# Optimization experiments

Measured on AMD Instinct MI355X. Metric: run time of the kernel, lower is better.

The kernel has to match this reference:

```python
import jax, jax.numpy as jnp
import numpy as np

N = 100000
NLAYERS = 4
NPROP = 2
NGRAPHS = 50


def gcn_conv(x, edge_index, W, b):
    """PyG GCNConv: h = x@W; out[d] = sum_e norm_e * h[src_e] (+ self loops), norm = D^-1/2 A_hat D^-1/2."""
    n = x.shape[0]
    loop = jnp.arange(n, dtype=edge_index.dtype)
    src = jnp.concatenate([edge_index[0], loop])
    dst = jnp.concatenate([edge_index[1], loop])
    deg = jax.ops.segment_sum(jnp.ones(src.shape[0], x.dtype), dst, num_segments=n)
    dinv = jax.lax.rsqrt(deg)  # deg >= 1 thanks to self loops
    norm = (dinv[src] * dinv[dst])[:, None]
    h = x @ W
    return jax.ops.segment_sum(h[src] * norm, dst, num_segments=n) + b


def setup_inputs() -> dict:
    key = jax.random.key(0)
    ks = jax.random.split(key, 16)
    inp = {
        "x": jax.random.normal(ks[0], (N, 16), jnp.float32),
        "feature_mtx_static": jax.random.normal(ks[1], (N, 32), jnp.float32),
        "edge_index": jax.random.randint(ks[2], (2, 400000), 0, N, jnp.int32),
        "inner_edges": jax.random.randint(ks[3], (NLAYERS, 2, 300000), 0, N, jnp.int32),
        "forward_edges": jax.random.randint(ks[4], (NLAYERS, 2, 300000), 0, N, jnp.int32),
        "backward_edges": jax.random.randint(ks[5], (NLAYERS, 2, 300000), 0, N, jnp.int32),
        "layers": jax.random.randint(ks[6], (N,), 0, NLAYERS, jnp.int32),
        "batch": jnp.sort(jax.random.randint(ks[7], (N,), 0, NGRAPHS, jnp.int32)),
        "W_up": jax.random.normal(ks[8], (16, 256), jnp.float32) * 0.25,
        "b_up": jax.random.normal(ks[9], (256,), jnp.float32) * 0.02,
        "W_in": jax.random.normal(ks[10], (288, 256), jnp.float32) * 0.06,
        "b_in": jax.random.normal(ks[11], (256,), jnp.float32) * 0.02,
        "W_fw": jax.random.normal(ks[12], (288, 256), jnp.float32) * 0.06,
        "b_fw": jax.random.normal(ks[13], (256,), jnp.float32) * 0.02,
        "W_lin": jax.random.normal(ks[14], (256, 1), jnp.float32) * 0.06,
        "b_lin": jax.random.normal(ks[15], (1,), jnp.float32) * 0.02,
    }
    return inp


def reference(x, feature_mtx_static, edge_index, inner_edges, forward_edges,
              backward_edges, layers, batch, W_up, b_up, W_in, b_in,
              W_fw, b_fw, W_lin, b_lin):
    def addstatic(h):
        return jnp.concatenate([h, feature_mtx_static], axis=1)

    x = gcn_conv(x, edge_index, W_up, b_up)
    partial_inner = x  # placeholder; overwritten in forward sweep
    for _ in range(NPROP):
        for il in range(NLAYERS):
            layermask = layers == il
            partial_inner = gcn_conv(addstatic(x), inner_edges[il], W_in, b_in)
            x = jnp.where(layermask[:, None], partial_inner, x)
            next_layer_mask = layers == il + 1
            partial_forward = gcn_conv(addstatic(x), forward_edges[il], W_fw, b_fw)
            x = jnp.where(next_layer_mask[:, None], partial_forward, x)
        x = jax.nn.relu(x)
        for il in range(NLAYERS - 1, -1, -1):
            # NOTE: original code computes forward_conv on backward_edges here but
            # assigns from the stale `partial_inner` (dead compute skipped).
            previous_layer_mask = layers == il - 1
            x = jnp.where(previous_layer_mask[:, None], partial_inner, x)
            layermask = layers == il
            partial_backward = gcn_conv(addstatic(x), inner_edges[il], W_in, b_in)
            x = jnp.where(layermask[:, None], partial_backward, x)
        x = jax.nn.relu(x)

    pooled = jax.ops.segment_sum(x, batch, num_segments=NGRAPHS)  # [G, 256]
    return pooled @ W_lin + b_lin  # [G, 1]
```

## Files before the change

### kernel.cpp

```cpp
#include <hip/hip_runtime.h>

#define N_NODES 100000
#define NLAYERS 4
#define NPROP 2
#define NGRAPHS 50
#define NE_MAIN 400000
#define NE_SET 300000
#define NSETS 9
#define CSR_TOTAL (NE_MAIN + 8 * NE_SET)
#define ASTR 296
#define WFSZ (9 * 16 * 512)
#define PCHUNK 4096
#define NCHK 25

typedef __attribute__((ext_vector_type(8))) short bf8_t;
typedef __attribute__((ext_vector_type(8))) unsigned short us8_t;
typedef __attribute__((ext_vector_type(4))) float f4_t;

__device__ __align__(16) unsigned short g_x[(size_t)N_NODES * 256];
__device__ __align__(16) unsigned short g_pi[(size_t)N_NODES * 256];
__device__ __align__(16) unsigned short g_fsb[(size_t)N_NODES * 32];
__device__ __align__(16) float g_agg16[(size_t)N_NODES * 16];
__device__ __align__(16) float g_dinv[NSETS * N_NODES];
__device__ __align__(16) float g_pooled[NGRAPHS * 256];
__device__ __align__(16) unsigned short g_Wfh[2 * WFSZ];
__device__ __align__(16) unsigned short g_Wfl[2 * WFSZ];
__device__ int g_deg[NSETS * N_NODES];
__device__ int g_cur[NSETS * N_NODES];
__device__ int g_off[NSETS * (N_NODES + 1)];
__device__ int g_part[NSETS * NCHK];
__device__ int g_csrs[CSR_TOTAL];
__device__ int g_cnt[4];
__device__ int g_lists[NLAYERS * N_NODES];

__host__ __device__ inline int csr_base(int slot) {
    return slot == 0 ? 0 : NE_MAIN + (slot - 1) * NE_SET;
}

__device__ inline unsigned short f2bf(float f) {
    unsigned u = __float_as_uint(f);
    return (unsigned short)((u + 0x7fffu + ((u >> 16) & 1u)) >> 16);
}
__device__ inline float bf2f(unsigned short b) {
    return __uint_as_float(((unsigned)b) << 16);
}

__device__ inline void edge_decode(int t, const int* ei, const int* inner, const int* fwd,
                                   int& slot, const int*& es, const int*& ed, int& e) {
    if (t < NE_MAIN) {
        slot = 0; e = t; es = ei; ed = ei + NE_MAIN;
    } else {
        int r = t - NE_MAIN;
        int grp = r / NE_SET;
        e = r - grp * NE_SET;
        slot = 1 + grp;
        const int* base = (grp < 4) ? (inner + grp * 2 * NE_SET)
                                    : (fwd + (grp - 4) * 2 * NE_SET);
        es = base; ed = base + NE_SET;
    }
}


__global__ __launch_bounds__(256) void k_init() {
    int i = blockIdx.x * blockDim.x + threadIdx.x;
    if (i < NSETS * N_NODES) g_deg[i] = 0;
    if (i < NGRAPHS * 256) g_pooled[i] = 0.f;
    if (i < 4) g_cnt[i] = 0;
}

__global__ __launch_bounds__(256) void k_fsb(const float* __restrict__ fs) {
    int i = blockIdx.x * blockDim.x + threadIdx.x;
    if (i < N_NODES * 32) g_fsb[i] = f2bf(fs[i]);
}

__global__ __launch_bounds__(256) void k_count_all(const int* __restrict__ ei,
                                                   const int* __restrict__ inner,
                                                   const int* __restrict__ fwd) {
    int t = blockIdx.x * blockDim.x + threadIdx.x;
    if (t >= CSR_TOTAL) return;
    int slot, e; const int *es, *ed;
    edge_decode(t, ei, inner, fwd, slot, es, ed, e);
    atomicAdd(&g_deg[slot * N_NODES + ed[e]], 1);
}

__global__ __launch_bounds__(256) void k_dinv() {
    int i = blockIdx.x * blockDim.x + threadIdx.x;
    if (i < NSETS * N_NODES) g_dinv[i] = rsqrtf(1.0f + (float)g_deg[i]);
}

__global__ __launch_bounds__(256) void k_wt(const float* __restrict__ W, int which) {
    int t = blockIdx.x * blockDim.x + threadIdx.x;
    if (t >= 288 * 256) return;
    int k = t >> 8, n = t & 255;
    int kb = k >> 5, kq = k & 31, quad = kq >> 3, ke = kq & 7;
    int nt = n >> 4, m = n & 15, lane = quad * 16 + m;
    int idx = which * WFSZ + (kb * 16 + nt) * 512 + lane * 8 + ke;
    float w = W[t];
    unsigned short h = f2bf(w);
    unsigned short l = f2bf(w - bf2f(h));
    g_Wfh[idx] = h;
    g_Wfl[idx] = l;
}


__global__ __launch_bounds__(256) void k_scan_a() {
    int b = blockIdx.x;
    int set = b / NCHK, ch = b % NCHK;
    const int* deg = g_deg + (size_t)set * N_NODES;
    int base = ch * PCHUNK + threadIdx.x * 16;
    int s = 0;
#pragma unroll
    for (int j = 0; j < 16; j++) {
        int id = base + j;
        if (id < N_NODES) s += deg[id];
    }
    __shared__ int sm[256];
    sm[threadIdx.x] = s;
    __syncthreads();
    for (int o = 128; o > 0; o >>= 1) {
        if (threadIdx.x < o) sm[threadIdx.x] += sm[threadIdx.x + o];
        __syncthreads();
    }
    if (threadIdx.x == 0) g_part[b] = sm[0];
}

__global__ __launch_bounds__(1024) void k_scan_b() {
    int wv = threadIdx.x >> 6, lane = threadIdx.x & 63;
    if (wv >= NSETS) return;
    int v = (lane < NCHK) ? g_part[wv * NCHK + lane] : 0;
    int orig = v;
    for (int o = 1; o < 32; o <<= 1) {
        int u = __shfl_up(v, o);
        if (lane >= o) v += u;
    }
    if (lane < NCHK) g_part[wv * NCHK + lane] = v - orig;
}

__global__ __launch_bounds__(256) void k_scan_c() {
    int b = blockIdx.x;
    int set = b / NCHK, ch = b % NCHK;
    const int* deg = g_deg + (size_t)set * N_NODES;
    int* off = g_off + (size_t)set * (N_NODES + 1);
    int* cur = g_cur + (size_t)set * N_NODES;
    int t = threadIdx.x;
    int base = ch * PCHUNK + t * 16;
    int v[16];
    int s = 0;
#pragma unroll
    for (int j = 0; j < 16; j++) {
        int id = base + j;
        v[j] = (id < N_NODES) ? deg[id] : 0;
        s += v[j];
    }
    __shared__ int sm[256];
    sm[t] = s;
    __syncthreads();
    for (int o = 1; o < 256; o <<= 1) {
        int u = (t >= o) ? sm[t - o] : 0;
        __syncthreads();
        sm[t] += u;
        __syncthreads();
    }
    int run = g_part[b] + sm[t] - s;
#pragma unroll
    for (int j = 0; j < 16; j++) {
        int id = base + j;
        if (id < N_NODES) { off[id] = run; cur[id] = run; }
        run += v[j];
    }
    if (ch == NCHK - 1 && t == 255) off[N_NODES] = (set == 0) ? NE_MAIN : NE_SET;
}

__global__ __launch_bounds__(256) void k_fill_all(const int* __restrict__ ei,
                                                  const int* __restrict__ inner,
                                                  const int* __restrict__ fwd) {
    int t = blockIdx.x * blockDim.x + threadIdx.x;
    if (t >= CSR_TOTAL) return;
    int slot, e; const int *es, *ed;
    edge_decode(t, ei, inner, fwd, slot, es, ed, e);
    int s = es[e], d = ed[e];
    int pos = atomicAdd(&g_cur[slot * N_NODES + d], 1);
    g_csrs[csr_base(slot) + pos] = s;
}

__global__ __launch_bounds__(256) void k_lists(const int* __restrict__ layers) {
    __shared__ int lcnt[4];
    __shared__ int lbase[4];
    int i = blockIdx.x * blockDim.x + threadIdx.x;
    if (threadIdx.x < 4) lcnt[threadIdx.x] = 0;
    __syncthreads();
    int l = -1, p = 0;
    if (i < N_NODES) {
        l = layers[i];
        p = atomicAdd(&lcnt[l], 1);
    }
    __syncthreads();
    if (threadIdx.x < 4) lbase[threadIdx.x] = atomicAdd(&g_cnt[threadIdx.x], lcnt[threadIdx.x]);
    __syncthreads();
    if (l >= 0) g_lists[l * N_NODES + lbase[l] + p] = i;
}


__global__ __launch_bounds__(256) void k_gather16(const float* __restrict__ xin) {
    int g = blockIdx.x * blockDim.x + threadIdx.x;
    int i = g >> 4, lane = g & 15;
    if (i >= N_NODES) return;
    float dv = g_dinv[i];
    float acc = dv * dv * xin[i * 16 + lane];
    int e0 = g_off[i], e1 = g_off[i + 1];
    for (int e = e0; e < e1; e++) {
        int s = g_csrs[e];
        acc += g_dinv[s] * dv * xin[s * 16 + lane];
    }
    g_agg16[i * 16 + lane] = acc;
}

__global__ __launch_bounds__(256) void k_gemm0(const float* __restrict__ W,
                                               const float* __restrict__ bias) {
    __shared__ float a[128];
    int base = blockIdx.x * 8;
    int t = threadIdx.x;
    if (t < 128) a[t] = g_agg16[base * 16 + t];
    __syncthreads();
    float bb = bias[t];
    for (int r = 0; r < 8; r++) {
        float acc = bb;
#pragma unroll
        for (int k = 0; k < 16; k++) acc += a[r * 16 + k] * W[k * 256 + t];
        g_x[(size_t)(base + r) * 256 + t] = f2bf(acc);
    }
}


__global__ __launch_bounds__(256, 4) void k_conv(int slot, int which,
                                                 const float* __restrict__ bias,
                                                 const int* __restrict__ layersp,
                                                 int layer, int topi) {
    int count = (layer >= 0) ? g_cnt[layer] : N_NODES;
    int base = blockIdx.x * 32;
    if (base >= count) return;
    const unsigned short* Wfh = g_Wfh + (size_t)which * WFSZ;
    const unsigned short* Wfl = g_Wfl + (size_t)which * WFSZ;
    unsigned short* out = topi ? g_pi : g_x;

    __shared__ unsigned short lds_h[32 * ASTR];
    __shared__ unsigned short lds_l[32 * ASTR];
    __shared__ int rows_s[32];
    int t = threadIdx.x;
    if (t < 32) {
        int r = base + t;
        rows_s[t] = (r < count) ? ((layer >= 0) ? g_lists[layer * N_NODES + r] : r) : -1;
    }
    __syncthreads();

    int wv = t >> 6, lane = t & 63;
    int grp = lane >> 4, gl = lane & 15;

    const float* dinv_s = g_dinv + (size_t)slot * N_NODES;
    const int* offp = g_off + (size_t)slot * (N_NODES + 1);
    int cb = csr_base(slot);
    for (int rr = 0; rr < 2; rr++) {
        int lr = wv * 8 + grp * 2 + rr;
        int row = rows_s[lr];
        float acc0[8], acc1[8], accf[8];
#pragma unroll
        for (int j = 0; j < 8; j++) { acc0[j] = 0.f; acc1[j] = 0.f; accf[j] = 0.f; }
        if (row >= 0) {
            float dvr = dinv_s[row];
            float d2 = dvr * dvr;
            us8_t u0 = *(const us8_t*)&g_x[(size_t)row * 256 + gl * 8];
            us8_t u1 = *(const us8_t*)&g_x[(size_t)row * 256 + 128 + gl * 8];
#pragma unroll
            for (int j = 0; j < 8; j++) { acc0[j] = d2 * bf2f(u0[j]); acc1[j] = d2 * bf2f(u1[j]); }
            if (gl < 4) {
                us8_t uf = *(const us8_t*)&g_fsb[(size_t)row * 32 + gl * 8];
#pragma unroll
                for (int j = 0; j < 8; j++) accf[j] = d2 * bf2f(uf[j]);
            }
            int e0 = offp[row] + cb, e1e = offp[row + 1] + cb;
            int e = e0;
            for (; e + 1 < e1e; e += 2) {
                int sa = g_csrs[e], sb = g_csrs[e + 1];
                float na = dinv_s[sa] * dvr;
                float nb = dinv_s[sb] * dvr;
                us8_t va0 = *(const us8_t*)&g_x[(size_t)sa * 256 + gl * 8];
                us8_t va1 = *(const us8_t*)&g_x[(size_t)sa * 256 + 128 + gl * 8];
                us8_t vb0 = *(const us8_t*)&g_x[(size_t)sb * 256 + gl * 8];
                us8_t vb1 = *(const us8_t*)&g_x[(size_t)sb * 256 + 128 + gl * 8];
#pragma unroll
                for (int j = 0; j < 8; j++) {
                    acc0[j] += na * bf2f(va0[j]); acc1[j] += na * bf2f(va1[j]);
                    acc0[j] += nb * bf2f(vb0[j]); acc1[j] += nb * bf2f(vb1[j]);
                }
                if (gl < 4) {
                    us8_t fa = *(const us8_t*)&g_fsb[(size_t)sa * 32 + gl * 8];
                    us8_t fb = *(const us8_t*)&g_fsb[(size_t)sb * 32 + gl * 8];
#pragma unroll
                    for (int j = 0; j < 8; j++)
                        accf[j] += na * bf2f(fa[j]) + nb * bf2f(fb[j]);
                }
            }
            if (e < e1e) {
                int sa = g_csrs[e];
                float na = dinv_s[sa] * dvr;
                us8_t va0 = *(const us8_t*)&g_x[(size_t)sa * 256 + gl * 8];
                us8_t va1 = *(const us8_t*)&g_x[(size_t)sa * 256 + 128 + gl * 8];
#pragma unroll
                for (int j = 0; j < 8; j++) {
                    acc0[j] += na * bf2f(va0[j]); acc1[j] += na * bf2f(va1[j]);
                }
                if (gl < 4) {
                    us8_t fa = *(const us8_t*)&g_fsb[(size_t)sa * 32 + gl * 8];
#pragma unroll
                    for (int j = 0; j < 8; j++) accf[j] += na * bf2f(fa[j]);
                }
            }
        }
        us8_t h0, l0, h1, l1;
#pragma unroll
        for (int j = 0; j < 8; j++) {
            h0[j] = f2bf(acc0[j]); l0[j] = f2bf(acc0[j] - bf2f(h0[j]));
            h1[j] = f2bf(acc1[j]); l1[j] = f2bf(acc1[j] - bf2f(h1[j]));
        }
        *(us8_t*)&lds_h[lr * ASTR + gl * 8] = h0;
        *(us8_t*)&lds_h[lr * ASTR + 128 + gl * 8] = h1;
        *(us8_t*)&lds_l[lr * ASTR + gl * 8] = l0;
        *(us8_t*)&lds_l[lr * ASTR + 128 + gl * 8] = l1;
        if (gl < 4) {
            us8_t hf, lf;
#pragma unroll
            for (int j = 0; j < 8; j++) {
                hf[j] = f2bf(accf[j]); lf[j] = f2bf(accf[j] - bf2f(hf[j]));
            }
            *(us8_t*)&lds_h[lr * ASTR + 256 + gl * 8] = hf;
            *(us8_t*)&lds_l[lr * ASTR + 256 + gl * 8] = lf;
        }
    }
    __syncthreads();

    int m = lane & 15, quad = lane >> 4;
    int n0 = wv * 64;
    f4_t acc2[2][4];
#pragma unroll
    for (int rt = 0; rt < 2; rt++)
#pragma unroll
        for (int ct = 0; ct < 4; ct++) acc2[rt][ct] = (f4_t){0.f, 0.f, 0.f, 0.f};

    for (int kb = 0; kb < 9; kb++) {
        int k0 = kb * 32;
        bf8_t ah0 = *(const bf8_t*)&lds_h[m * ASTR + k0 + quad * 8];
        bf8_t al0 = *(const bf8_t*)&lds_l[m * ASTR + k0 + quad * 8];
        bf8_t ah1 = *(const bf8_t*)&lds_h[(16 + m) * ASTR + k0 + quad * 8];
        bf8_t al1 = *(const bf8_t*)&lds_l[(16 + m) * ASTR + k0 + quad * 8];
#pragma unroll
        for (int ct = 0; ct < 4; ct++) {
            int nt = wv * 4 + ct;
            const bf8_t bh = *(const bf8_t*)&Wfh[(kb * 16 + nt) * 512 + lane * 8];
            const bf8_t bl = *(const bf8_t*)&Wfl[(kb * 16 + nt) * 512 + lane * 8];
            acc2[0][ct] = __builtin_amdgcn_mfma_f32_16x16x32_bf16(ah0, bh, acc2[0][ct], 0, 0, 0);
            acc2[0][ct] = __builtin_amdgcn_mfma_f32_16x16x32_bf16(al0, bh, acc2[0][ct], 0, 0, 0);
            acc2[0][ct] = __builtin_amdgcn_mfma_f32_16x16x32_bf16(ah0, bl, acc2[0][ct], 0, 0, 0);
            acc2[1][ct] = __builtin_amdgcn_mfma_f32_16x16x32_bf16(ah1, bh, acc2[1][ct], 0, 0, 0);
            acc2[1][ct] = __builtin_amdgcn_mfma_f32_16x16x32_bf16(al1, bh, acc2[1][ct], 0, 0, 0);
            acc2[1][ct] = __builtin_amdgcn_mfma_f32_16x16x32_bf16(ah1, bl, acc2[1][ct], 0, 0, 0);
        }
    }
#pragma unroll
    for (int rt = 0; rt < 2; rt++) {
#pragma unroll
        for (int r = 0; r < 4; r++) {
            int row = rows_s[rt * 16 + quad * 4 + r];
            if (row < 0) continue;
            int dual = topi && (layersp[row] == 3);
#pragma unroll
            for (int ct = 0; ct < 4; ct++) {
                int n = n0 + ct * 16 + m;
                unsigned short v = f2bf(acc2[rt][ct][r] + bias[n]);
                out[(size_t)row * 256 + n] = v;
                if (dual) g_x[(size_t)row * 256 + n] = v;
            }
        }
    }
}


__global__ __launch_bounds__(256) void k_copy_rows(int layer) {
    int w = (blockIdx.x * blockDim.x + threadIdx.x) >> 5;
    int lane = threadIdx.x & 31;
    if (w >= g_cnt[layer]) return;
    int i = g_lists[layer * N_NODES + w];
    *(uint4*)(g_x + (size_t)i * 256 + lane * 8) =
        *(const uint4*)(g_pi + (size_t)i * 256 + lane * 8);
}

__global__ __launch_bounds__(256) void k_relu() {
    int i = blockIdx.x * blockDim.x + threadIdx.x;
    if (i >= N_NODES * 32) return;
    ushort4 a = ((ushort4*)g_x)[i * 2];
    ushort4 b = ((ushort4*)g_x)[i * 2 + 1];
    a.x = (a.x & 0x8000) ? 0 : a.x; a.y = (a.y & 0x8000) ? 0 : a.y;
    a.z = (a.z & 0x8000) ? 0 : a.z; a.w = (a.w & 0x8000) ? 0 : a.w;
    b.x = (b.x & 0x8000) ? 0 : b.x; b.y = (b.y & 0x8000) ? 0 : b.y;
    b.z = (b.z & 0x8000) ? 0 : b.z; b.w = (b.w & 0x8000) ? 0 : b.w;
    ((ushort4*)g_x)[i * 2] = a;
    ((ushort4*)g_x)[i * 2 + 1] = b;
}

__global__ __launch_bounds__(256) void k_pool(const int* __restrict__ batch) {
    __shared__ int bs[128];
    int i0 = blockIdx.x * 128;
    if (threadIdx.x < 128) {
        int i = i0 + threadIdx.x;
        bs[threadIdx.x] = (i < N_NODES) ? batch[i] : -1;
    }
    __syncthreads();
    int c = threadIdx.x;
    int lim = min(128, N_NODES - i0);
    float acc = 0.f;
    int cur = bs[0];
    for (int ii = 0; ii < lim; ii++) {
        int g = bs[ii];
        if (g != cur) { atomicAdd(&g_pooled[cur * 256 + c], acc); acc = 0.f; cur = g; }
        acc += fmaxf(bf2f(g_x[(size_t)(i0 + ii) * 256 + c]), 0.f);
    }
    atomicAdd(&g_pooled[cur * 256 + c], acc);
}

__global__ void k_final(const float* __restrict__ W_lin, const float* __restrict__ b_lin,
                        float* __restrict__ out) {
    int g = blockIdx.x;
    int lane = threadIdx.x;
    float4 p = *(const float4*)(g_pooled + g * 256 + lane * 4);
    float4 w = *(const float4*)(W_lin + lane * 4);
    float s = p.x * w.x + p.y * w.y + p.z * w.z + p.w * w.w;
    for (int o = 32; o > 0; o >>= 1) s += __shfl_down(s, o);
    if (lane == 0) out[g] = s + b_lin[0];
}


extern "C" void kernel_launch(void* const* d_in, const int* in_sizes, int n_in,
                              void* d_out, int out_size, void* d_ws, size_t ws_size,
                              hipStream_t stream) {
    const float* xin   = (const float*)d_in[0];
    const float* fs    = (const float*)d_in[1];
    const int* ei      = (const int*)d_in[2];
    const int* inner   = (const int*)d_in[3];
    const int* fwd     = (const int*)d_in[4];
    const int* layers  = (const int*)d_in[6];
    const int* batch   = (const int*)d_in[7];
    const float* W_up  = (const float*)d_in[8];
    const float* b_up  = (const float*)d_in[9];
    const float* W_in  = (const float*)d_in[10];
    const float* b_in  = (const float*)d_in[11];
    const float* W_fw  = (const float*)d_in[12];
    const float* b_fw  = (const float*)d_in[13];
    const float* W_lin = (const float*)d_in[14];
    const float* b_lin = (const float*)d_in[15];
    float* out = (float*)d_out;

    k_init<<<(NSETS * N_NODES + 255) / 256, 256, 0, stream>>>();
    k_fsb<<<(N_NODES * 32 + 255) / 256, 256, 0, stream>>>(fs);
    k_wt<<<(288 * 256 + 255) / 256, 256, 0, stream>>>(W_in, 0);
    k_wt<<<(288 * 256 + 255) / 256, 256, 0, stream>>>(W_fw, 1);
    k_count_all<<<(CSR_TOTAL + 255) / 256, 256, 0, stream>>>(ei, inner, fwd);
    k_dinv<<<(NSETS * N_NODES + 255) / 256, 256, 0, stream>>>();
    k_scan_a<<<NSETS * NCHK, 256, 0, stream>>>();
    k_scan_b<<<1, 1024, 0, stream>>>();
    k_scan_c<<<NSETS * NCHK, 256, 0, stream>>>();
    k_fill_all<<<(CSR_TOTAL + 255) / 256, 256, 0, stream>>>(ei, inner, fwd);
    k_lists<<<(N_NODES + 255) / 256, 256, 0, stream>>>(layers);

    k_gather16<<<(N_NODES * 16 + 255) / 256, 256, 0, stream>>>(xin);
    k_gemm0<<<N_NODES / 8, 256, 0, stream>>>(W_up, b_up);

    auto conv = [&](int slot, int which, const float* bias, int layer, int topi) {
        k_conv<<<(N_NODES + 31) / 32, 256, 0, stream>>>(slot, which, bias, layers, layer, topi);
    };

    for (int p = 0; p < NPROP; p++) {
        for (int il = 0; il < NLAYERS; il++) {
            if (il < NLAYERS - 1) {
                conv(1 + il, 0, b_in, il, 0);
                conv(5 + il, 1, b_fw, il + 1, 0);
            } else {
                conv(1 + il, 0, b_in, -1, 1);
            }
        }
        k_relu<<<(N_NODES * 32 + 255) / 256, 256, 0, stream>>>();
        for (int il = NLAYERS - 1; il >= 0; il--) {
            if (il >= 1) k_copy_rows<<<12500, 256, 0, stream>>>(il - 1);
            conv(1 + il, 0, b_in, il, 0);
        }
        if (p < NPROP - 1)
            k_relu<<<(N_NODES * 32 + 255) / 256, 256, 0, stream>>>();
    }

    k_pool<<<(N_NODES + 127) / 128, 256, 0, stream>>>(batch);
    k_final<<<NGRAPHS, 64, 0, stream>>>(W_lin, b_lin, out);
}
```

Baseline: 1.508 ms.

## Build filtered CSR containing only edges for destination rows actually consumed

```diff
diff --git a/kernel.cpp b/kernel.cpp
--- a/kernel.cpp
+++ b/kernel.cpp
@@ -26,6 +26,7 @@
 __device__ __align__(16) unsigned short g_Wfh[2 * WFSZ];
 __device__ __align__(16) unsigned short g_Wfl[2 * WFSZ];
 __device__ int g_deg[NSETS * N_NODES];
+__device__ int g_degf[NSETS * N_NODES];
 __device__ int g_cur[NSETS * N_NODES];
 __device__ int g_off[NSETS * (N_NODES + 1)];
 __device__ int g_part[NSETS * NCHK];
@@ -60,10 +61,17 @@
     }
 }
 
+__device__ inline int csr_keep(int slot, int ld) {
+    if (slot == 0 || slot == 4) return 1;
+    if (slot <= 3) return ld == slot - 1;
+    if (slot <= 7) return ld == slot - 4;
+    return 0;
+}
+
 
 __global__ __launch_bounds__(256) void k_init() {
     int i = blockIdx.x * blockDim.x + threadIdx.x;
-    if (i < NSETS * N_NODES) g_deg[i] = 0;
+    if (i < NSETS * N_NODES) { g_deg[i] = 0; g_degf[i] = 0; }
     if (i < NGRAPHS * 256) g_pooled[i] = 0.f;
     if (i < 4) g_cnt[i] = 0;
 }
@@ -75,12 +83,16 @@
 
 __global__ __launch_bounds__(256) void k_count_all(const int* __restrict__ ei,
                                                    const int* __restrict__ inner,
-                                                   const int* __restrict__ fwd) {
+                                                   const int* __restrict__ fwd,
+                                                   const int* __restrict__ layers) {
     int t = blockIdx.x * blockDim.x + threadIdx.x;
-    if (t >= CSR_TOTAL) return;
+    if (t >= CSR_TOTAL - NE_SET) return;
     int slot, e; const int *es, *ed;
     edge_decode(t, ei, inner, fwd, slot, es, ed, e);
-    atomicAdd(&g_deg[slot * N_NODES + ed[e]], 1);
+    int d = ed[e];
+    atomicAdd(&g_deg[slot * N_NODES + d], 1);
+    if (slot == 0 || slot == 4 || csr_keep(slot, layers[d]))
+        atomicAdd(&g_degf[slot * N_NODES + d], 1);
 }
 
 __global__ __launch_bounds__(256) void k_dinv() {
@@ -106,7 +118,7 @@
 __global__ __launch_bounds__(256) void k_scan_a() {
     int b = blockIdx.x;
     int set = b / NCHK, ch = b % NCHK;
-    const int* deg = g_deg + (size_t)set * N_NODES;
+    const int* deg = g_degf + (size_t)set * N_NODES;
     int base = ch * PCHUNK + threadIdx.x * 16;
     int s = 0;
 #pragma unroll
@@ -139,7 +151,7 @@
 __global__ __launch_bounds__(256) void k_scan_c() {
     int b = blockIdx.x;
     int set = b / NCHK, ch = b % NCHK;
-    const int* deg = g_deg + (size_t)set * N_NODES;
+    const int* deg = g_degf + (size_t)set * N_NODES;
     int* off = g_off + (size_t)set * (N_NODES + 1);
     int* cur = g_cur + (size_t)set * N_NODES;
     int t = threadIdx.x;
@@ -168,17 +180,19 @@
         if (id < N_NODES) { off[id] = run; cur[id] = run; }
         run += v[j];
     }
-    if (ch == NCHK - 1 && t == 255) off[N_NODES] = (set == 0) ? NE_MAIN : NE_SET;
 }
 
 __global__ __launch_bounds__(256) void k_fill_all(const int* __restrict__ ei,
                                                   const int* __restrict__ inner,
-                                                  const int* __restrict__ fwd) {
+                                                  const int* __restrict__ fwd,
+                                                  const int* __restrict__ layers) {
     int t = blockIdx.x * blockDim.x + threadIdx.x;
-    if (t >= CSR_TOTAL) return;
+    if (t >= CSR_TOTAL - NE_SET) return;
     int slot, e; const int *es, *ed;
     edge_decode(t, ei, inner, fwd, slot, es, ed, e);
-    int s = es[e], d = ed[e];
+    int d = ed[e];
+    if (!(slot == 0 || slot == 4 || csr_keep(slot, layers[d]))) return;
+    int s = es[e];
     int pos = atomicAdd(&g_cur[slot * N_NODES + d], 1);
     g_csrs[csr_base(slot) + pos] = s;
 }
@@ -207,7 +221,7 @@
     if (i >= N_NODES) return;
     float dv = g_dinv[i];
     float acc = dv * dv * xin[i * 16 + lane];
-    int e0 = g_off[i], e1 = g_off[i + 1];
+    int e0 = g_off[i], e1 = g_off[i] + g_degf[i];
     for (int e = e0; e < e1; e++) {
         int s = g_csrs[e];
         acc += g_dinv[s] * dv * xin[s * 16 + lane];
@@ -234,7 +248,6 @@
 
 __global__ __launch_bounds__(256, 4) void k_conv(int slot, int which,
                                                  const float* __restrict__ bias,
-                                                 const int* __restrict__ layersp,
                                                  int layer, int topi) {
     int count = (layer >= 0) ? g_cnt[layer] : N_NODES;
     int base = blockIdx.x * 32;
@@ -258,6 +271,7 @@
 
     const float* dinv_s = g_dinv + (size_t)slot * N_NODES;
     const int* offp = g_off + (size_t)slot * (N_NODES + 1);
+    const int* degfp = g_degf + (size_t)slot * N_NODES;
     int cb = csr_base(slot);
     for (int rr = 0; rr < 2; rr++) {
         int lr = wv * 8 + grp * 2 + rr;
@@ -277,7 +291,7 @@
 #pragma unroll
                 for (int j = 0; j < 8; j++) accf[j] = d2 * bf2f(uf[j]);
             }
-            int e0 = offp[row] + cb, e1e = offp[row + 1] + cb;
+            int e0 = offp[row] + cb, e1e = e0 + degfp[row];
             int e = e0;
             for (; e + 1 < e1e; e += 2) {
                 int sa = g_csrs[e], sb = g_csrs[e + 1];
@@ -371,13 +385,10 @@
         for (int r = 0; r < 4; r++) {
             int row = rows_s[rt * 16 + quad * 4 + r];
             if (row < 0) continue;
-            int dual = topi && (layersp[row] == 3);
 #pragma unroll
             for (int ct = 0; ct < 4; ct++) {
                 int n = n0 + ct * 16 + m;
-                unsigned short v = f2bf(acc2[rt][ct][r] + bias[n]);
-                out[(size_t)row * 256 + n] = v;
-                if (dual) g_x[(size_t)row * 256 + n] = v;
+                out[(size_t)row * 256 + n] = f2bf(acc2[rt][ct][r] + bias[n]);
             }
         }
     }
@@ -462,19 +473,19 @@
     k_fsb<<<(N_NODES * 32 + 255) / 256, 256, 0, stream>>>(fs);
     k_wt<<<(288 * 256 + 255) / 256, 256, 0, stream>>>(W_in, 0);
     k_wt<<<(288 * 256 + 255) / 256, 256, 0, stream>>>(W_fw, 1);
-    k_count_all<<<(CSR_TOTAL + 255) / 256, 256, 0, stream>>>(ei, inner, fwd);
+    k_count_all<<<(CSR_TOTAL - NE_SET + 255) / 256, 256, 0, stream>>>(ei, inner, fwd, layers);
     k_dinv<<<(NSETS * N_NODES + 255) / 256, 256, 0, stream>>>();
     k_scan_a<<<NSETS * NCHK, 256, 0, stream>>>();
     k_scan_b<<<1, 1024, 0, stream>>>();
     k_scan_c<<<NSETS * NCHK, 256, 0, stream>>>();
-    k_fill_all<<<(CSR_TOTAL + 255) / 256, 256, 0, stream>>>(ei, inner, fwd);
+    k_fill_all<<<(CSR_TOTAL - NE_SET + 255) / 256, 256, 0, stream>>>(ei, inner, fwd, layers);
     k_lists<<<(N_NODES + 255) / 256, 256, 0, stream>>>(layers);
 
     k_gather16<<<(N_NODES * 16 + 255) / 256, 256, 0, stream>>>(xin);
     k_gemm0<<<N_NODES / 8, 256, 0, stream>>>(W_up, b_up);
 
     auto conv = [&](int slot, int which, const float* bias, int layer, int topi) {
-        k_conv<<<(N_NODES + 31) / 32, 256, 0, stream>>>(slot, which, bias, layers, layer, topi);
+        k_conv<<<(N_NODES + 31) / 32, 256, 0, stream>>>(slot, which, bias, layer, topi);
     };
 
     for (int p = 0; p < NPROP; p++) {
@@ -484,6 +495,7 @@
                 conv(5 + il, 1, b_fw, il + 1, 0);
             } else {
                 conv(1 + il, 0, b_in, -1, 1);
+                k_copy_rows<<<12500, 256, 0, stream>>>(3);
             }
         }
         k_relu<<<(N_NODES * 32 + 255) / 256, 256, 0, stream>>>();
```

New measurement: 1.366 ms. -9.4%, faster.
